# Optimization experiments

Measured on AMD Instinct MI355X. Metric: run time of the kernel, lower is better.

## Reference

```python
import jax, jax.numpy as jnp
import numpy as np

N_WAY = 5
K_SHOT = 5
TEMPERATURE = 0.2
EPS = 1e-12  # torch F.normalize eps


def setup_inputs() -> dict:
    key = jax.random.key(0)
    k1, k2, k3, k4 = jax.random.split(key, 4)
    b, q, c, h, w = 4, 75, 640, 10, 10
    s = N_WAY * K_SHOT
    return {
        "support_xf": jax.random.normal(k1, (b, s, c, h, w), dtype=jnp.float32),
        "support_y": jax.random.randint(k2, (b, s), 0, N_WAY),
        "query_xf": jax.random.normal(k3, (b, q, c, h, w), dtype=jnp.float32),
        "query_y": jax.random.randint(k4, (b, q), 0, N_WAY),
    }


def _l2norm(x):
    # normalize along last axis (channel), matching F.normalize semantics
    n = jnp.sqrt(jnp.sum(x * x, axis=-1, keepdims=True))
    return x / jnp.maximum(n, EPS)


def _inner_simi(support_xf, query_xf):
    # cosine similarity between all query local descriptors and all support
    # local descriptors, grouped per class -> [b, q, N, M_q, M_s]
    b, s, c, h, w = support_xf.shape
    q = query_xf.shape[1]
    hw = h * w
    Ms = K_SHOT * hw
    sx = support_xf.reshape(b, N_WAY, K_SHOT, c, hw)
    sx = jnp.transpose(sx, (0, 1, 2, 4, 3)).reshape(b, N_WAY, Ms, c)  # [b,N,M_s,c]
    qx = jnp.transpose(query_xf.reshape(b, q, c, hw), (0, 1, 3, 2))  # [b,q,M_q,c]
    return jnp.einsum('bqmc,bnsc->bqnms', _l2norm(qx), _l2norm(sx))


def _dmnn_mask(simi):
    # simi: [b,q,N,M_q,M_s] -> bool mask [b,q,M_q]
    b, q, N, Mq, Ms = simi.shape
    merged = jnp.transpose(simi, (0, 1, 3, 2, 4)).reshape(b, q, Mq, N * Ms)
    query_nearest = jnp.argmax(merged, axis=-1)            # [b,q,M_q] global NN idx
    class_max = jnp.max(simi, axis=-1)                      # [b,q,N,M_q]
    top2 = jax.lax.top_k(jnp.transpose(class_max, (0, 1, 3, 2)), 2)[0]  # [b,q,M_q,2]
    query_class_diff = top2[..., 0] - top2[..., 1]          # [b,q,M_q]
    diffs_m = jax.nn.one_hot(query_nearest, N * Ms, dtype=simi.dtype) \
        * query_class_diff[..., None]                       # [b,q,M_q,N*M_s]
    diffs_max_nearest = jnp.argmax(diffs_m, axis=-2)        # [b,q,N*M_s]
    gathered = jnp.take_along_axis(diffs_max_nearest, query_nearest, axis=-1)  # [b,q,M_q]
    return gathered == jnp.arange(Mq)[None, None, :]


def reference(support_xf, support_y, query_xf, query_y):
    b, q = query_xf.shape[0], query_xf.shape[1]
    simi = _inner_simi(support_xf, query_xf)                # [b,q,N,M_q,M_s]
    q_mask = _dmnn_mask(simi)                               # [b,q,M_q]
    class_max = jnp.max(simi, axis=-1)                      # [b,q,N,M_q]
    query_value = jnp.sum(class_max * q_mask[:, :, None, :].astype(simi.dtype), axis=-1)
    logits = query_value.reshape(b * q, N_WAY) / TEMPERATURE
    logp = jax.nn.log_softmax(logits, axis=-1)
    labels = query_y.reshape(b * q)
    loss = -jnp.mean(jnp.take_along_axis(logp, labels[:, None], axis=1))
    return loss
```

## Files before the change

kernel.cpp:

```cpp
#include <hip/hip_runtime.h>
#include <math.h>

#define B 4
#define Q 75
#define NBQ (B*Q)
#define NWAY 5
#define KSHOT 5
#define C 640
#define HW 100
#define MS 500
#define SLAB (C*HW)

#define MT32_B 236
#define RT_B 472
#define A_CHUNKS_B (RT_B*20*64)
#define S_CHUNKS_ALL (20*32*20*64)
#define S_CHUNKS_B   (5*32*20*64)

#define CHI 0.00390625f
#define CLO 1.9073486328125e-06f

typedef _Float16 half8 __attribute__((ext_vector_type(8)));
typedef float f32x4 __attribute__((ext_vector_type(4)));

__device__ __forceinline__ void gl_lds16(const void* gsrc, void* ldst) {
  __builtin_amdgcn_global_load_lds(
      (const __attribute__((address_space(1))) unsigned int*)gsrc,
      (__attribute__((address_space(3))) unsigned int*)ldst, 16, 0, 0);
}

#define WS_BASE 340352ull
#define NEED_ALL   104908288ull
#define NEED_PERB   46908928ull
#define NEED_PERB2  27248128ull

__global__ __launch_bounds__(256) void norm_kernel(const float* __restrict__ s_xf,
                                                   const float* __restrict__ q_xf,
                                                   float* __restrict__ invs,
                                                   float* __restrict__ invq) {
  int id = blockIdx.x;
  const float* base;
  float* out;
  if (id < 100) { base = s_xf + (size_t)id * SLAB;        out = invs + id * HW; }
  else          { base = q_xf + (size_t)(id - 100) * SLAB; out = invq + (id - 100) * HW; }
  __shared__ float ssum[2][HW];
  int t = threadIdx.x;
  if (t < 2 * HW) ((float*)ssum)[t] = 0.f;
  __syncthreads();
  if (t < 2 * HW) {
    int p = t % HW, half = t / HW;
    float part = 0.f;
    for (int ch = half * 320; ch < half * 320 + 320; ++ch) {
      float v = base[ch * HW + p];
      part = fmaf(v, v, part);
    }
    ssum[half][p] = part;
  }
  __syncthreads();
  if (t < HW) {
    float nrm = sqrtf(ssum[0][t] + ssum[1][t]);
    out[t] = 1.f / fmaxf(nrm, 1e-12f);
  }
}

__device__ __forceinline__ void dual_split(float w, _Float16* h0, _Float16* h1) {
  _Float16 a = (_Float16)w;
  *h0 = a;
  *h1 = (_Float16)((w - (float)a) * 2048.f);
}

__global__ __launch_bounds__(256) void convs_kernel(const float* __restrict__ s_xf,
                                                    const float* __restrict__ invs,
                                                    uint4* __restrict__ o0,
                                                    uint4* __restrict__ o1,
                                                    int bn0) {
  int id = blockIdx.x * 256 + threadIdx.x;
  int lane = id & 63;
  int tmp = id >> 6;
  int ks = tmp % 20;
  int t2 = tmp / 20;
  int jf = t2 % 32;
  int bnl = t2 / 32;
  int bn = bn0 + bnl;
  int j = jf * 16 + (lane & 15);
  int k = ks * 32 + (lane >> 4) * 8;
  union { _Float16 h[8]; uint4 u; } p0, p1;
  if (j < MS) {
    int s = j / 100, p = j % 100;
    int slab = bn * 5 + s;
    const float* src = s_xf + ((size_t)slab * 640 + k) * 100 + p;
    float sc = invs[slab * 100 + p] * 16.f;
#pragma unroll
    for (int kj = 0; kj < 8; ++kj)
      dual_split(src[kj * 100] * sc, &p0.h[kj], &p1.h[kj]);
  } else {
    p0.u = make_uint4(0, 0, 0, 0);
    p1.u = make_uint4(0, 0, 0, 0);
  }
  o0[id] = p0.u; o1[id] = p1.u;
}

__global__ __launch_bounds__(256) void convq_kernel(const float* __restrict__ q_xf,
                                                    const float* __restrict__ invq,
                                                    uint4* __restrict__ o0,
                                                    uint4* __restrict__ o1,
                                                    int b0) {
  int id = blockIdx.x * 256 + threadIdx.x;
  int bloc = id / A_CHUNKS_B;
  int c = id % A_CHUNKS_B;
  int bb = b0 + bloc;
  int lane = c & 63;
  int tmp = c >> 6;
  int ks = tmp % 20;
  int rt = tmp / 20;
  int row = rt * 16 + (lane & 15);
  int k = ks * 32 + (lane >> 4) * 8;
  union { _Float16 h[8]; uint4 u; } p0, p1;
  if (row < Q * HW) {
    int qi = row / 100, p = row % 100;
    const float* src = q_xf + ((size_t)(bb * Q + qi) * 640 + k) * 100 + p;
    float sc = invq[(bb * Q + qi) * 100 + p] * 16.f;
#pragma unroll
    for (int kj = 0; kj < 8; ++kj)
      dual_split(src[kj * 100] * sc, &p0.h[kj], &p1.h[kj]);
  } else {
    p0.u = make_uint4(0, 0, 0, 0);
    p1.u = make_uint4(0, 0, 0, 0);
  }
  o0[id] = p0.u; o1[id] = p1.u;
}

__global__ __launch_bounds__(256, 3) void gemm_kernel(
    const uint4* __restrict__ a0, const uint4* __restrict__ a1,
    const uint4* __restrict__ b0p, const uint4* __restrict__ b1p,
    float* __restrict__ cmax, int* __restrict__ carg,
    int bq0, int aStride, int sbnBase, int mode ) {
  int wgid = blockIdx.x;
  int x = wgid & 7, s = wgid >> 3;
  int o;
  if (mode == 0) {
    o = x * 590 + s;
  } else {
    if (x < 4) { if (s >= 148) return; o = x * 148 + s; }
    else       { if (s >= 147) return; o = 592 + (x - 4) * 147 + s; }
  }
  int bnloc = o / MT32_B;
  int mt32 = o % MT32_B;
  int bloc = bnloc / 5;
  int n = bnloc % 5;
  int bb = bq0 + bloc;
  const uint4* A0 = a0 + (size_t)bloc * aStride;
  const uint4* A1 = a1 + (size_t)bloc * aStride;
  int bnl = bb * 5 + n - sbnBase;

  __shared__ __align__(16) _Float16 sA[2][2][2][512];
  __shared__ float sV[4][32];
  __shared__ int   sJ[4][32];

  int t = threadIdx.x;
  int w = t >> 6, lane = t & 63;

  if (lane < 32) { sV[w][lane] = -1e30f; sJ[w][lane] = 0; }

#define STAGE_A1(KS, BUF) do {                                                  \
    int limb_ = w >> 1, rtl_ = w & 1;                                           \
    size_t aIdx = ((size_t)(mt32 * 2 + rtl_) * 20 + (KS)) * 64 + lane;          \
    gl_lds16((limb_ ? A1 : A0) + aIdx, (void*)&sA[(BUF)][limb_][rtl_][0]);      \
  } while (0)

#define MFMA_STEP(BV0, BV1, BUF) do {                                           \
    _Pragma("unroll")                                                           \
    for (int mf = 0; mf < 2; ++mf) {                                            \
      half8 av0 = *(const half8*)&sA[(BUF)][0][mf][lane * 8];                   \
      half8 av1 = *(const half8*)&sA[(BUF)][1][mf][lane * 8];                   \
      _Pragma("unroll")                                                         \
      for (int f = 0; f < 4; ++f) {                                             \
        acc0[mf][f] = __builtin_amdgcn_mfma_f32_16x16x32_f16(av0, BV0[f], acc0[mf][f], 0, 0, 0); \
        accM[mf][f] = __builtin_amdgcn_mfma_f32_16x16x32_f16(av0, BV1[f], accM[mf][f], 0, 0, 0); \
        accM[mf][f] = __builtin_amdgcn_mfma_f32_16x16x32_f16(av1, BV0[f], accM[mf][f], 0, 0, 0); \
      }                                                                         \
    }                                                                           \
  } while (0)

  for (int pass = 0; pass < 2; ++pass) {
    int jf0 = pass * 16 + w * 4;
    size_t bBase = (size_t)(bnl * 32 + jf0) * 1280 + lane;

    f32x4 acc0[2][4], accM[2][4];
#pragma unroll
    for (int mf = 0; mf < 2; ++mf)
#pragma unroll
      for (int f = 0; f < 4; ++f) {
        acc0[mf][f] = (f32x4){0.f, 0.f, 0.f, 0.f};
        accM[mf][f] = (f32x4){0.f, 0.f, 0.f, 0.f};
      }

    half8 bE0[4], bE1[4], bO0[4], bO1[4];
#pragma unroll
    for (int f = 0; f < 4; ++f) bE0[f] = *(const half8*)&b0p[bBase + (size_t)f * 1280];
#pragma unroll
    for (int f = 0; f < 4; ++f) bE1[f] = *(const half8*)&b1p[bBase + (size_t)f * 1280];
    STAGE_A1(0, 0);

#pragma unroll 1
    for (int kk = 0; kk < 10; ++kk) {
      __syncthreads();
      {
        size_t bo = bBase + (size_t)(2 * kk + 1) * 64;
#pragma unroll
        for (int f = 0; f < 4; ++f) bO0[f] = *(const half8*)&b0p[bo + (size_t)f * 1280];
#pragma unroll
        for (int f = 0; f < 4; ++f) bO1[f] = *(const half8*)&b1p[bo + (size_t)f * 1280];
      }
      STAGE_A1(2 * kk + 1, 1);
      __builtin_amdgcn_sched_barrier(0);
      MFMA_STEP(bE0, bE1, 0);

      __syncthreads();
      if (kk < 9) {
        size_t bo = bBase + (size_t)(2 * kk + 2) * 64;
#pragma unroll
        for (int f = 0; f < 4; ++f) bE0[f] = *(const half8*)&b0p[bo + (size_t)f * 1280];
#pragma unroll
        for (int f = 0; f < 4; ++f) bE1[f] = *(const half8*)&b1p[bo + (size_t)f * 1280];
        STAGE_A1(2 * kk + 2, 0);
      }
      __builtin_amdgcn_sched_barrier(0);
      MFMA_STEP(bO0, bO1, 1);
    }

#pragma unroll
    for (int mf = 0; mf < 2; ++mf)
#pragma unroll
      for (int f = 0; f < 4; ++f) {
        int j = pass * 256 + w * 64 + f * 16 + (lane & 15);
        bool ok = (j < MS);
#pragma unroll
        for (int rg = 0; rg < 4; ++rg) {
          float v = ok ? (acc0[mf][f][rg] * CHI + accM[mf][f][rg] * CLO) : -1e30f;
          int ji = ok ? j : 0x7fffffff;
#pragma unroll
          for (int mk = 1; mk < 16; mk <<= 1) {
            float ov = __shfl_xor(v, mk);
            int oj = __shfl_xor(ji, mk);
            if (ov > v || (ov == v && oj < ji)) { v = ov; ji = oj; }
          }
          if ((lane & 15) == 0) {
            int row32 = mf * 16 + (lane >> 4) * 4 + rg;
            if (v > sV[w][row32]) { sV[w][row32] = v; sJ[w][row32] = ji; }
          }
        }
      }
  }
#undef STAGE_A1
#undef MFMA_STEP

  __syncthreads();
  if (w == 0 && lane < 32) {
    int row32 = lane;
    float v = sV[0][row32];
    int ji = sJ[0][row32];
#pragma unroll
    for (int q4 = 1; q4 < 4; ++q4) {
      float ov = sV[q4][row32];
      int oj = sJ[q4][row32];
      if (ov > v || (ov == v && oj < ji)) { v = ov; ji = oj; }
    }
    int r = mt32 * 32 + row32;
    if (r < Q * HW) {
      int bq = bb * Q + r / 100, p = r % 100;
      size_t oo = (size_t)(bq * NWAY + n) * HW + p;
      cmax[oo] = v;
      carg[oo] = ji;
    }
  }
}

#define TCF 32
#define TJF 64
__global__ __launch_bounds__(256) void simi_kernel(const float* __restrict__ s_xf,
                                                   const float* __restrict__ q_xf,
                                                   const float* __restrict__ invs,
                                                   const float* __restrict__ invq,
                                                   float* __restrict__ cmax,
                                                   int* __restrict__ carg) {
  int id = blockIdx.x;
  int n = id % NWAY;
  int bq = id / NWAY;
  int b = bq / Q;
  const float* qbase = q_xf + (size_t)bq * SLAB;
  const float* sbase = s_xf + (size_t)(b * 25 + n * KSHOT) * SLAB;
  const float* invqB = invq + bq * HW;
  const float* invsB = invs + (b * 2500 + n * MS);

  __shared__ __align__(16) float As[TCF][112];
  __shared__ __align__(16) float Bs[TCF][TJF];
  __shared__ float sInvQ[HW];
  __shared__ float sInvS[MS];

  int t = threadIdx.x;
  for (int i = t; i < HW; i += 256) sInvQ[i] = invqB[i];
  for (int i = t; i < MS; i += 256) sInvS[i] = invsB[i];

  int tj = t & 15, tm = t >> 4;
  float best[7];
  int bidx[7];
#pragma unroll
  for (int r = 0; r < 7; ++r) { best[r] = -1e30f; bidx[r] = 0; }

  for (int jt0 = 0; jt0 < MS; jt0 += TJF) {
    float acc[7][4];
#pragma unroll
    for (int r = 0; r < 7; ++r)
#pragma unroll
      for (int jj = 0; jj < 4; ++jj) acc[r][jj] = 0.f;
    for (int c0 = 0; c0 < C; c0 += TCF) {
      __syncthreads();
      for (int i = t; i < TCF * HW; i += 256) {
        int p = i % HW;
        As[i / HW][p] = qbase[c0 * HW + i] * sInvQ[p];
      }
      for (int i = t; i < TCF * TJF; i += 256) {
        int cc = i / TJF, jj = i % TJF;
        int j = jt0 + jj;
        float v = 0.f;
        if (j < MS) v = sbase[(j / 100) * SLAB + (c0 + cc) * 100 + (j % 100)] * sInvS[j];
        Bs[cc][jj] = v;
      }
      __syncthreads();
#pragma unroll
      for (int cc = 0; cc < TCF; ++cc) {
        float4 bv = *(const float4*)&Bs[cc][tj * 4];
#pragma unroll
        for (int r = 0; r < 7; ++r) {
          float a = As[cc][tm * 7 + r];
          acc[r][0] = fmaf(a, bv.x, acc[r][0]);
          acc[r][1] = fmaf(a, bv.y, acc[r][1]);
          acc[r][2] = fmaf(a, bv.z, acc[r][2]);
          acc[r][3] = fmaf(a, bv.w, acc[r][3]);
        }
      }
    }
#pragma unroll
    for (int r = 0; r < 7; ++r)
#pragma unroll
      for (int jj = 0; jj < 4; ++jj) {
        int j = jt0 + tj * 4 + jj;
        float v = acc[r][jj];
        if (j < MS && v > best[r]) { best[r] = v; bidx[r] = j; }
      }
  }
#pragma unroll
  for (int r = 0; r < 7; ++r)
#pragma unroll
    for (int mask = 1; mask < 16; mask <<= 1) {
      float ov = __shfl_xor(best[r], mask);
      int oi = __shfl_xor(bidx[r], mask);
      if (ov > best[r] || (ov == best[r] && oi < bidx[r])) { best[r] = ov; bidx[r] = oi; }
    }
  if (tj == 0)
#pragma unroll
    for (int r = 0; r < 7; ++r) {
      int m = tm * 7 + r;
      if (m < HW) {
        cmax[(size_t)(bq * NWAY + n) * HW + m] = best[r];
        carg[(size_t)(bq * NWAY + n) * HW + m] = bidx[r];
      }
    }
}

__global__ __launch_bounds__(128) void mask_loss_kernel(const float* __restrict__ cmax,
                                                        const int* __restrict__ carg,
                                                        const int* __restrict__ query_y,
                                                        float* __restrict__ lossv) {
  int bq = blockIdx.x;
  int t = threadIdx.x;
  __shared__ float sDiff[HW];
  __shared__ int sNear[HW];
  __shared__ float sCm[NWAY][HW];
  __shared__ float red[128];

  if (t < HW) {
    float cm[NWAY];
#pragma unroll
    for (int nn = 0; nn < NWAY; ++nn) {
      cm[nn] = cmax[(size_t)(bq * NWAY + nn) * HW + t];
      sCm[nn][t] = cm[nn];
    }
    float v0 = -1e30f, v1 = -1e30f;
#pragma unroll
    for (int nn = 0; nn < NWAY; ++nn) {
      float v = cm[nn];
      if (v > v0) { v1 = v0; v0 = v; }
      else if (v > v1) { v1 = v; }
    }
    sDiff[t] = v0 - v1;
    float gb = -1e30f;
    int gn = 0;
#pragma unroll
    for (int nn = 0; nn < NWAY; ++nn)
      if (cm[nn] > gb) { gb = cm[nn]; gn = nn; }
    sNear[t] = gn * MS + carg[(size_t)(bq * NWAY + gn) * HW + t];
  }
  __syncthreads();

  bool msk = false;
  if (t < HW) {
    int j = sNear[t];
    int wn = 0;
    float wv = -1.f;
    for (int mp = 0; mp < HW; ++mp) {
      float v = (sNear[mp] == j) ? sDiff[mp] : 0.f;
      if (v > wv) { wv = v; wn = mp; }
    }
    msk = (wn == t);
  }

  float qv[NWAY];
#pragma unroll
  for (int nn = 0; nn < NWAY; ++nn) {
    __syncthreads();
    red[t] = (t < HW && msk) ? sCm[nn][t] : 0.f;
    __syncthreads();
    for (int s = 64; s > 0; s >>= 1) {
      if (t < s) red[t] += red[t + s];
      __syncthreads();
    }
    qv[nn] = red[0];
  }

  if (t == 0) {
    float logits[NWAY], mx = -1e30f;
#pragma unroll
    for (int nn = 0; nn < NWAY; ++nn) {
      logits[nn] = qv[nn] / 0.2f;
      mx = fmaxf(mx, logits[nn]);
    }
    float se = 0.f;
#pragma unroll
    for (int nn = 0; nn < NWAY; ++nn) se += expf(logits[nn] - mx);
    float lse = mx + logf(se);
    int label = query_y[bq];
    lossv[bq] = -(logits[label] - lse);
  }
}

__global__ __launch_bounds__(512) void finalize_kernel(const float* __restrict__ lossv,
                                                       float* __restrict__ out) {
  __shared__ float red[512];
  int t = threadIdx.x;
  red[t] = (t < NBQ) ? lossv[t] : 0.f;
  __syncthreads();
  for (int s = 256; s > 0; s >>= 1) {
    if (t < s) red[t] += red[t + s];
    __syncthreads();
  }
  if (t == 0) out[0] = red[0] / (float)NBQ;
}

extern "C" void kernel_launch(void* const* d_in, const int* in_sizes, int n_in,
                              void* d_out, int out_size, void* d_ws, size_t ws_size,
                              hipStream_t stream) {
  const float* s_xf = (const float*)d_in[0];
  const float* q_xf = (const float*)d_in[2];
  const int* query_y = (const int*)d_in[3];

  float* ws = (float*)d_ws;
  float* invs = ws;
  float* invq = ws + 10000;
  float* cmax = ws + 40000;
  int* carg = (int*)(ws + 190000);
  float* lossv = ws + 340000;

  norm_kernel<<<400, 256, 0, stream>>>(s_xf, q_xf, invs, invq);

  const size_t SP_ALL = 3276800, SP_B = 819200, QS_B = 2416640;

  if (ws_size >= NEED_ALL) {
    uint4* S0 = (uint4*)(ws + WS_BASE);
    uint4* S1 = (uint4*)(ws + WS_BASE + SP_ALL);
    uint4* Q0 = (uint4*)(ws + WS_BASE + 2 * SP_ALL);
    uint4* Q1 = (uint4*)(ws + WS_BASE + 2 * SP_ALL + 4 * QS_B);
    convs_kernel<<<S_CHUNKS_ALL / 256, 256, 0, stream>>>(s_xf, invs, S0, S1, 0);
    convq_kernel<<<4 * A_CHUNKS_B / 256, 256, 0, stream>>>(q_xf, invq, Q0, Q1, 0);
    gemm_kernel<<<4720, 256, 0, stream>>>(Q0, Q1, S0, S1,
                                          cmax, carg, 0, A_CHUNKS_B, 0, 0);
  } else if (ws_size >= NEED_PERB) {
    uint4* S0 = (uint4*)(ws + WS_BASE);
    uint4* S1 = (uint4*)(ws + WS_BASE + SP_ALL);
    uint4* Q0 = (uint4*)(ws + WS_BASE + 2 * SP_ALL);
    uint4* Q1 = (uint4*)(ws + WS_BASE + 2 * SP_ALL + QS_B);
    convs_kernel<<<S_CHUNKS_ALL / 256, 256, 0, stream>>>(s_xf, invs, S0, S1, 0);
    for (int b = 0; b < 4; ++b) {
      convq_kernel<<<A_CHUNKS_B / 256, 256, 0, stream>>>(q_xf, invq, Q0, Q1, b);
      gemm_kernel<<<1184, 256, 0, stream>>>(Q0, Q1, S0, S1,
                                            cmax, carg, b, 0, 0, 1);
    }
  } else if (ws_size >= NEED_PERB2) {
    uint4* S0 = (uint4*)(ws + WS_BASE);
    uint4* S1 = (uint4*)(ws + WS_BASE + SP_B);
    uint4* Q0 = (uint4*)(ws + WS_BASE + 2 * SP_B);
    uint4* Q1 = (uint4*)(ws + WS_BASE + 2 * SP_B + QS_B);
    for (int b = 0; b < 4; ++b) {
      convs_kernel<<<S_CHUNKS_B / 256, 256, 0, stream>>>(s_xf, invs, S0, S1, b * 5);
      convq_kernel<<<A_CHUNKS_B / 256, 256, 0, stream>>>(q_xf, invq, Q0, Q1, b);
      gemm_kernel<<<1184, 256, 0, stream>>>(Q0, Q1, S0, S1,
                                            cmax, carg, b, 0, b * 5, 1);
    }
  } else {
    simi_kernel<<<1500, 256, 0, stream>>>(s_xf, q_xf, invs, invq, cmax, carg);
  }

  mask_loss_kernel<<<NBQ, 128, 0, stream>>>(cmax, carg, query_y, lossv);
  finalize_kernel<<<1, 512, 0, stream>>>(lossv, (float*)d_out);
}
```

Baseline: 541.0 us.

## Deepen A-tile LDS pipeline to four buffers with partial vmcnt waits

Changes the A-operand shared-memory staging from double to quad buffering and prefetches three k-steps ahead. Full __syncthreads are replaced with barriers that wait only on the older outstanding loads via s_waitcnt vmcnt. The aim is to hide global-to-LDS latency behind the MFMAs and cut barrier stalls. In exchange it doubles sA LDS usage, issues clamped redundant loads at the tail, and depends on exact counts of in-flight loads, which breaks if the compiler reorders them.

```diff
diff --git a/kernel.cpp b/kernel.cpp
--- a/kernel.cpp
+++ b/kernel.cpp
@@ -153,7 +153,7 @@
   const uint4* A1 = a1 + (size_t)bloc * aStride;
   int bnl = bb * 5 + n - sbnBase;
 
-  __shared__ __align__(16) _Float16 sA[2][2][2][512];
+  __shared__ __align__(16) _Float16 sA[4][2][2][512];
   __shared__ float sV[4][32];
   __shared__ int   sJ[4][32];
 
@@ -162,11 +162,12 @@
 
   if (lane < 32) { sV[w][lane] = -1e30f; sJ[w][lane] = 0; }
 
-#define STAGE_A1(KS, BUF) do {                                                  \
-    int limb_ = w >> 1, rtl_ = w & 1;                                           \
-    size_t aIdx = ((size_t)(mt32 * 2 + rtl_) * 20 + (KS)) * 64 + lane;          \
-    gl_lds16((limb_ ? A1 : A0) + aIdx, (void*)&sA[(BUF)][limb_][rtl_][0]);      \
-  } while (0)
+  int limb_ = w >> 1, rtl_ = w & 1;
+  const uint4* Asrc = limb_ ? A1 : A0;
+  size_t aRow = (size_t)(mt32 * 2 + rtl_) * 20;
+
+#define STAGE_A1(KS, BUF) \
+    gl_lds16(Asrc + (aRow + (KS)) * 64 + lane, (void*)&sA[(BUF)][limb_][rtl_][0])
 
 #define MFMA_STEP(BV0, BV1, BUF) do {                                           \
     _Pragma("unroll")                                                           \
@@ -182,7 +183,15 @@
     }                                                                           \
   } while (0)
 
+#define END_BARRIER() do {                                                      \
+    asm volatile("s_waitcnt vmcnt(10)" ::: "memory");                           \
+    __builtin_amdgcn_sched_barrier(0);                                          \
+    __builtin_amdgcn_s_barrier();                                               \
+    __builtin_amdgcn_sched_barrier(0);                                          \
+  } while (0)
+
   for (int pass = 0; pass < 2; ++pass) {
+    __syncthreads();
     int jf0 = pass * 16 + w * 4;
     size_t bBase = (size_t)(bnl * 32 + jf0) * 1280 + lane;
 
@@ -201,32 +210,42 @@
 #pragma unroll
     for (int f = 0; f < 4; ++f) bE1[f] = *(const half8*)&b1p[bBase + (size_t)f * 1280];
     STAGE_A1(0, 0);
+    STAGE_A1(1, 1);
+    STAGE_A1(2, 2);
+    asm volatile("s_waitcnt vmcnt(2)" ::: "memory");
+    __builtin_amdgcn_sched_barrier(0);
+    __builtin_amdgcn_s_barrier();
+    __builtin_amdgcn_sched_barrier(0);
 
 #pragma unroll 1
     for (int kk = 0; kk < 10; ++kk) {
-      __syncthreads();
+      int ks = 2 * kk;
       {
-        size_t bo = bBase + (size_t)(2 * kk + 1) * 64;
+        size_t bo = bBase + (size_t)(ks + 1) * 64;
 #pragma unroll
         for (int f = 0; f < 4; ++f) bO0[f] = *(const half8*)&b0p[bo + (size_t)f * 1280];
 #pragma unroll
         for (int f = 0; f < 4; ++f) bO1[f] = *(const half8*)&b1p[bo + (size_t)f * 1280];
-      }
-      STAGE_A1(2 * kk + 1, 1);
+        int ka = (ks + 3 > 19) ? 19 : ks + 3;
+        STAGE_A1(ka, (ks + 3) & 3);
+      }
       __builtin_amdgcn_sched_barrier(0);
-      MFMA_STEP(bE0, bE1, 0);
-
-      __syncthreads();
-      if (kk < 9) {
-        size_t bo = bBase + (size_t)(2 * kk + 2) * 64;
+      MFMA_STEP(bE0, bE1, ks & 3);
+      END_BARRIER();
+
+      {
+        int kb = (ks + 2 > 19) ? 19 : ks + 2;
+        size_t bo = bBase + (size_t)kb * 64;
 #pragma unroll
         for (int f = 0; f < 4; ++f) bE0[f] = *(const half8*)&b0p[bo + (size_t)f * 1280];
 #pragma unroll
         for (int f = 0; f < 4; ++f) bE1[f] = *(const half8*)&b1p[bo + (size_t)f * 1280];
-        STAGE_A1(2 * kk + 2, 0);
+        int ka = (ks + 4 > 19) ? 19 : ks + 4;
+        STAGE_A1(ka, (ks + 4) & 3);
       }
       __builtin_amdgcn_sched_barrier(0);
-      MFMA_STEP(bO0, bO1, 1);
+      MFMA_STEP(bO0, bO1, (ks + 1) & 3);
+      END_BARRIER();
     }
 
 #pragma unroll
@@ -254,6 +273,7 @@
   }
 #undef STAGE_A1
 #undef MFMA_STEP
+#undef END_BARRIER
 
   __syncthreads();
   if (w == 0 && lane < 32) {
```

After: 570.7 us. +5.5%, slower.
